# Kernel tuning notes

Hardware: AMD Instinct MI355X
Metric: run time of the kernel (lower is better)

The kernel has to match this reference:

```python
import jax, jax.numpy as jnp
import numpy as np

N_NODES = 50000


def gcn_conv(x, edge_index, W, b):
    # PyG GCNConv: h = X @ W; add self-loops; sym-normalize; scatter-add to target; + bias
    N = x.shape[0]
    h = x @ W
    src = jnp.concatenate([edge_index[0], jnp.arange(N)])
    dst = jnp.concatenate([edge_index[1], jnp.arange(N)])
    ew = jnp.ones(src.shape[0], dtype=h.dtype)
    deg = jax.ops.segment_sum(ew, dst, num_segments=N)
    dinv = jnp.where(deg > 0, deg ** -0.5, 0.0)
    norm = dinv[src] * ew * dinv[dst]              # [E+N]
    msg = h[src] * norm[:, None]                   # gather + scale
    out = jax.ops.segment_sum(msg, dst, num_segments=N)  # scatter-add
    return out + b


def setup_inputs() -> dict:
    key = jax.random.key(0)
    ks = jax.random.split(key, 8)
    x = jax.random.normal(ks[0], (N_NODES, 128), dtype=jnp.float32)
    edge_index = jax.random.randint(ks[1], (2, 800000), 0, N_NODES)
    W1 = jax.random.normal(ks[2], (128, 96), dtype=jnp.float32) * 0.1
    b1 = jax.random.normal(ks[3], (96,), dtype=jnp.float32) * 0.1
    W_mu = jax.random.normal(ks[4], (96, 64), dtype=jnp.float32) * 0.1
    b_mu = jax.random.normal(ks[5], (64,), dtype=jnp.float32) * 0.1
    W_lv = jax.random.normal(ks[6], (96, 64), dtype=jnp.float32) * 0.1
    b_lv = jax.random.normal(ks[7], (64,), dtype=jnp.float32) * 0.1
    return {"x": x, "edge_index": edge_index, "W1": W1, "b1": b1,
            "W_mu": W_mu, "b_mu": b_mu, "W_lv": W_lv, "b_lv": b_lv}


def reference(x, edge_index, W1, b1, W_mu, b_mu, W_lv, b_lv):
    h = jax.nn.relu(gcn_conv(x, edge_index, W1, b1))
    mu = gcn_conv(h, edge_index, W_mu, b_mu).sum(axis=0, keepdims=True)      # SumAggregation -> [1, out]
    logvar = gcn_conv(h, edge_index, W_lv, b_lv).sum(axis=0, keepdims=True)  # [1, out]
    return (mu, logvar)
```

## Files before the change

### kernel.cpp

```cpp
#include <hip/hip_runtime.h>
#include <hip/hip_fp16.h>


#define NCHUNK 32
#define LOG_NCHUNK 5
#define NSLICE 16
#define SLICE_MAX 3136
#define SORT_T 1024

typedef float v2f __attribute__((ext_vector_type(2)));

__device__ inline void fma4(float4& c, float a, const float4& b) {
    c.x = fmaf(a, b.x, c.x); c.y = fmaf(a, b.y, c.y);
    c.z = fmaf(a, b.z, c.z); c.w = fmaf(a, b.w, c.w);
}

__device__ inline unsigned pk_fp8(float a, float b, float c, float d) {
    int p = __builtin_amdgcn_cvt_pk_fp8_f32(a, b, 0, false);
    p = __builtin_amdgcn_cvt_pk_fp8_f32(c, d, p, true);
    return (unsigned)p;
}

__device__ inline void add_fp8(float4& acc, unsigned u) {
    v2f f;
    f = __builtin_amdgcn_cvt_pk_f32_fp8(u, false); acc.x += f.x; acc.y += f.y;
    f = __builtin_amdgcn_cvt_pk_f32_fp8(u, true);  acc.z += f.x; acc.w += f.y;
}

__launch_bounds__(SORT_T)
__global__ void k_count(const int* __restrict__ dst, unsigned short* __restrict__ pcount,
                        int N, int E, int chunkE, int sliceN) {
    int c = blockIdx.x & (NCHUNK - 1), s = blockIdx.x >> LOG_NCHUNK;
    int nbase = s * sliceN;
    __shared__ int hist[SLICE_MAX];
    for (int j = threadIdx.x; j < sliceN; j += SORT_T) hist[j] = 0;
    __syncthreads();
    int e0 = c * chunkE, e1 = min(e0 + chunkE, E);
    int ne = e1 - e0;
    const int4* d4 = (const int4*)(dst + e0);
    int n4 = ne >> 2;
    for (int i = threadIdx.x; i < n4; i += SORT_T) {
        int4 d = d4[i];
        unsigned q;
        q = (unsigned)(d.x - nbase); if (q < (unsigned)sliceN) atomicAdd(&hist[q], 1);
        q = (unsigned)(d.y - nbase); if (q < (unsigned)sliceN) atomicAdd(&hist[q], 1);
        q = (unsigned)(d.z - nbase); if (q < (unsigned)sliceN) atomicAdd(&hist[q], 1);
        q = (unsigned)(d.w - nbase); if (q < (unsigned)sliceN) atomicAdd(&hist[q], 1);
    }
    if (threadIdx.x < (ne & 3)) {
        int d = dst[e0 + (n4 << 2) + threadIdx.x];
        unsigned q = (unsigned)(d - nbase);
        if (q < (unsigned)sliceN) atomicAdd(&hist[q], 1);
    }
    __syncthreads();
    for (int j = threadIdx.x; j < sliceN; j += SORT_T) {
        int n = nbase + j;
        if (n < N) pcount[(size_t)c * N + n] = (unsigned short)hist[j];
    }
}

__launch_bounds__(256)
__global__ void k_degdinv(const unsigned short* __restrict__ pcount, int* __restrict__ deg,
                          float* __restrict__ dinv, int* __restrict__ blocksum, int N) {
    int tid = threadIdx.x;
    int n = blockIdx.x * 256 + tid;
    int s = 0;
    if (n < N) {
        #pragma unroll
        for (int c = 0; c < NCHUNK; ++c) s += pcount[(size_t)c * N + n];
        deg[n] = s;
        dinv[n] = rsqrtf((float)(s + 1));
    }
    __shared__ int sh[256];
    sh[tid] = s;
    __syncthreads();
    #pragma unroll
    for (int off = 128; off; off >>= 1) {
        if (tid < off) sh[tid] += sh[tid + off];
        __syncthreads();
    }
    if (tid == 0) blocksum[blockIdx.x] = sh[0];
}

__launch_bounds__(256)
__global__ void k_offs(const unsigned short* __restrict__ pcount, int* __restrict__ offs,
                       const int* __restrict__ deg, const int* __restrict__ blocksum,
                       int* __restrict__ rowptr, int N, int E, int nb) {
    int tid = threadIdx.x;
    __shared__ int sh[256];
    int bs = (tid < nb && tid < (int)blockIdx.x) ? blocksum[tid] : 0;
    sh[tid] = bs;
    __syncthreads();
    #pragma unroll
    for (int off = 128; off; off >>= 1) {
        if (tid < off) sh[tid] += sh[tid + off];
        __syncthreads();
    }
    int blockoff = sh[0];
    __syncthreads();
    int n = blockIdx.x * 256 + tid;
    int v = (n < N) ? deg[n] : 0;
    sh[tid] = v;
    __syncthreads();
    for (int off = 1; off < 256; off <<= 1) {
        int t = (tid >= off) ? sh[tid - off] : 0;
        __syncthreads();
        sh[tid] += t;
        __syncthreads();
    }
    int run = blockoff + sh[tid] - v;
    if (n < N) {
        rowptr[n] = run;
        #pragma unroll
        for (int c = 0; c < NCHUNK; ++c) {
            size_t ix = (size_t)c * N + n;
            int t = pcount[ix];
            offs[ix] = run;
            run += t;
        }
    }
    if (blockIdx.x == 0 && tid == 0) rowptr[N] = E;
}

__launch_bounds__(SORT_T)
__global__ void k_place(const int* __restrict__ src, const int* __restrict__ dst,
                        const float* __restrict__ dinv, int* __restrict__ offs,
                        int* __restrict__ col, int N, int E, int chunkE, int sliceN) {
    int c = blockIdx.x & (NCHUNK - 1), s = blockIdx.x >> LOG_NCHUNK;
    int nbase = s * sliceN;
    __shared__ int cur[SLICE_MAX];
    __shared__ float rs[SLICE_MAX];
    for (int j = threadIdx.x; j < sliceN; j += SORT_T) {
        int n = nbase + j;
        cur[j] = (n < N) ? offs[(size_t)c * N + n] : 0;
        rs[j] = 0.f;
    }
    __syncthreads();
    int e0 = c * chunkE, e1 = min(e0 + chunkE, E);
    int ne = e1 - e0;
    const int4* s4 = (const int4*)(src + e0);
    const int4* d4 = (const int4*)(dst + e0);
    int n4 = ne >> 2;
    for (int i = threadIdx.x; i < n4; i += SORT_T) {
        int4 sv = s4[i];
        int4 dv = d4[i];
        unsigned qd, qs;
        qd = (unsigned)(dv.x - nbase);
        if (qd < (unsigned)sliceN) { int p = atomicAdd(&cur[qd], 1); col[p] = sv.x; }
        qs = (unsigned)(sv.x - nbase);
        if (qs < (unsigned)sliceN) atomicAdd(&rs[qs], dinv[dv.x]);
        qd = (unsigned)(dv.y - nbase);
        if (qd < (unsigned)sliceN) { int p = atomicAdd(&cur[qd], 1); col[p] = sv.y; }
        qs = (unsigned)(sv.y - nbase);
        if (qs < (unsigned)sliceN) atomicAdd(&rs[qs], dinv[dv.y]);
        qd = (unsigned)(dv.z - nbase);
        if (qd < (unsigned)sliceN) { int p = atomicAdd(&cur[qd], 1); col[p] = sv.z; }
        qs = (unsigned)(sv.z - nbase);
        if (qs < (unsigned)sliceN) atomicAdd(&rs[qs], dinv[dv.z]);
        qd = (unsigned)(dv.w - nbase);
        if (qd < (unsigned)sliceN) { int p = atomicAdd(&cur[qd], 1); col[p] = sv.w; }
        qs = (unsigned)(sv.w - nbase);
        if (qs < (unsigned)sliceN) atomicAdd(&rs[qs], dinv[dv.w]);
    }
    if (threadIdx.x < (ne & 3)) {
        int e = e0 + (n4 << 2) + threadIdx.x;
        int sv = src[e], dv = dst[e];
        unsigned qd = (unsigned)(dv - nbase);
        if (qd < (unsigned)sliceN) { int p = atomicAdd(&cur[qd], 1); col[p] = sv; }
        unsigned qs = (unsigned)(sv - nbase);
        if (qs < (unsigned)sliceN) atomicAdd(&rs[qs], dinv[dv]);
    }
    __syncthreads();
    float* prs = (float*)offs;
    for (int j = threadIdx.x; j < sliceN; j += SORT_T) {
        int n = nbase + j;
        if (n < N) prs[(size_t)c * N + n] = rs[j];
    }
}

__launch_bounds__(256)
__global__ void k_gemm(const float* __restrict__ x, const float* __restrict__ W1,
                       const float* __restrict__ dinv, const float* __restrict__ prs,
                       float* __restrict__ cfac, unsigned* __restrict__ g, int n) {
    __shared__ float Ws[128 * 96];
    int tid = threadIdx.x;
    {
        const float4* wsrc = (const float4*)W1;
        float4* wdst = (float4*)Ws;
        #pragma unroll
        for (int i = 0; i < 12; ++i) wdst[tid + 256 * i] = wsrc[tid + 256 * i];
    }
    {
        int r = blockIdx.x * 128 + tid;
        if (tid < 128 && r < n) {
            float s = 0.f;
            #pragma unroll
            for (int c = 0; c < NCHUNK; ++c) s += prs[(size_t)c * n + r];
            float dv = dinv[r];
            cfac[r] = dv * (dv + s);
        }
    }
    __syncthreads();

    int tx = tid & 7;
    int ty = tid >> 3;
    int rbase = blockIdx.x * 128 + ty * 4;
    const float4* xp[4];
    bool vr[4];
    #pragma unroll
    for (int i = 0; i < 4; ++i) {
        int r = rbase + i;
        vr[i] = r < n;
        xp[i] = (const float4*)(x + (size_t)(vr[i] ? r : 0) * 128);
    }

    float4 acc[4][3];
    #pragma unroll
    for (int i = 0; i < 4; ++i)
        #pragma unroll
        for (int j = 0; j < 3; ++j) acc[i][j] = make_float4(0.f, 0.f, 0.f, 0.f);

    #pragma unroll 2
    for (int k4 = 0; k4 < 32; ++k4) {
        float4 a0 = xp[0][k4];
        float4 a1 = xp[1][k4];
        float4 a2 = xp[2][k4];
        float4 a3 = xp[3][k4];
        #pragma unroll
        for (int kk = 0; kk < 4; ++kk) {
            const float* wrow = &Ws[(k4 * 4 + kk) * 96 + tx * 12];
            float4 b0 = *(const float4*)(wrow);
            float4 b1 = *(const float4*)(wrow + 4);
            float4 b2 = *(const float4*)(wrow + 8);
            float av0 = (kk == 0) ? a0.x : (kk == 1) ? a0.y : (kk == 2) ? a0.z : a0.w;
            float av1 = (kk == 0) ? a1.x : (kk == 1) ? a1.y : (kk == 2) ? a1.z : a1.w;
            float av2 = (kk == 0) ? a2.x : (kk == 1) ? a2.y : (kk == 2) ? a2.z : a2.w;
            float av3 = (kk == 0) ? a3.x : (kk == 1) ? a3.y : (kk == 2) ? a3.z : a3.w;
            fma4(acc[0][0], av0, b0); fma4(acc[0][1], av0, b1); fma4(acc[0][2], av0, b2);
            fma4(acc[1][0], av1, b0); fma4(acc[1][1], av1, b1); fma4(acc[1][2], av1, b2);
            fma4(acc[2][0], av2, b0); fma4(acc[2][1], av2, b1); fma4(acc[2][2], av2, b2);
            fma4(acc[3][0], av3, b0); fma4(acc[3][1], av3, b1); fma4(acc[3][2], av3, b2);
        }
    }

    #pragma unroll
    for (int i = 0; i < 4; ++i) {
        if (!vr[i]) continue;
        int r = rbase + i;
        float dv = dinv[r] * 16.f;
        unsigned* o = g + (size_t)r * 24 + tx * 3;
        float4 t;
        t = acc[i][0]; o[0] = pk_fp8(t.x * dv, t.y * dv, t.z * dv, t.w * dv);
        t = acc[i][1]; o[1] = pk_fp8(t.x * dv, t.y * dv, t.z * dv, t.w * dv);
        t = acc[i][2]; o[2] = pk_fp8(t.x * dv, t.y * dv, t.z * dv, t.w * dv);
    }
}

#define AGG_NODES 16
#define AGG_T (AGG_NODES * 24)
__launch_bounds__(AGG_T)
__global__ void k_agg(const unsigned* __restrict__ g1, const int* __restrict__ col,
                      const int* __restrict__ rowptr, const float* __restrict__ dinv,
                      const float* __restrict__ cfac, const float* __restrict__ b1,
                      float* __restrict__ v_part, int n) {
    int tid = threadIdx.x;
    int nl = tid / 24;
    int ch = tid % 24;
    int d = blockIdx.x * AGG_NODES + nl;

    __shared__ float4 sh[AGG_NODES][24];

    float4 contrib = make_float4(0.f, 0.f, 0.f, 0.f);
    if (d < n) {
        float dds = dinv[d] * 0.0625f;
        int e0 = rowptr[d], e1 = rowptr[d + 1];
        float4 aA = make_float4(0.f, 0.f, 0.f, 0.f);
        float4 aB = make_float4(0.f, 0.f, 0.f, 0.f);
        float4 aC = make_float4(0.f, 0.f, 0.f, 0.f);
        float4 aD = make_float4(0.f, 0.f, 0.f, 0.f);
        int e = e0;
        for (; e + 8 <= e1; e += 8) {
            int s0 = __builtin_nontemporal_load(col + e);
            int s1 = __builtin_nontemporal_load(col + e + 1);
            int s2 = __builtin_nontemporal_load(col + e + 2);
            int s3 = __builtin_nontemporal_load(col + e + 3);
            int s4 = __builtin_nontemporal_load(col + e + 4);
            int s5 = __builtin_nontemporal_load(col + e + 5);
            int s6 = __builtin_nontemporal_load(col + e + 6);
            int s7 = __builtin_nontemporal_load(col + e + 7);
            unsigned u0 = g1[(size_t)s0 * 24 + ch];
            unsigned u1 = g1[(size_t)s1 * 24 + ch];
            unsigned u2 = g1[(size_t)s2 * 24 + ch];
            unsigned u3 = g1[(size_t)s3 * 24 + ch];
            unsigned u4 = g1[(size_t)s4 * 24 + ch];
            unsigned u5 = g1[(size_t)s5 * 24 + ch];
            unsigned u6 = g1[(size_t)s6 * 24 + ch];
            unsigned u7 = g1[(size_t)s7 * 24 + ch];
            add_fp8(aA, u0); add_fp8(aB, u1); add_fp8(aC, u2); add_fp8(aD, u3);
            add_fp8(aA, u4); add_fp8(aB, u5); add_fp8(aC, u6); add_fp8(aD, u7);
        }
        for (; e + 2 <= e1; e += 2) {
            int s0 = __builtin_nontemporal_load(col + e);
            int s1 = __builtin_nontemporal_load(col + e + 1);
            unsigned u0 = g1[(size_t)s0 * 24 + ch];
            unsigned u1 = g1[(size_t)s1 * 24 + ch];
            add_fp8(aA, u0); add_fp8(aB, u1);
        }
        if (e < e1) {
            int s0 = __builtin_nontemporal_load(col + e);
            add_fp8(aC, g1[(size_t)s0 * 24 + ch]);
        }
        add_fp8(aD, g1[(size_t)d * 24 + ch]);
        float4 b1c = ((const float4*)b1)[ch];
        float cd = cfac[d];
        float hx = fmaxf(fmaf(dds, (aA.x + aB.x) + (aC.x + aD.x), b1c.x), 0.f);
        float hy = fmaxf(fmaf(dds, (aA.y + aB.y) + (aC.y + aD.y), b1c.y), 0.f);
        float hz = fmaxf(fmaf(dds, (aA.z + aB.z) + (aC.z + aD.z), b1c.z), 0.f);
        float hw = fmaxf(fmaf(dds, (aA.w + aB.w) + (aC.w + aD.w), b1c.w), 0.f);
        contrib = make_float4(cd * hx, cd * hy, cd * hz, cd * hw);
    }
    sh[nl][ch] = contrib;
    __syncthreads();
    #pragma unroll
    for (int off = 8; off >= 1; off >>= 1) {
        if (nl < off) {
            float4 a = sh[nl][ch];
            float4 b = sh[nl + off][ch];
            a.x += b.x; a.y += b.y; a.z += b.z; a.w += b.w;
            sh[nl][ch] = a;
        }
        __syncthreads();
    }
    if (tid < 24) {
        ((float4*)(v_part + (size_t)blockIdx.x * 96))[tid] = sh[0][tid];
    }
}

__global__ void k_vred(const float* __restrict__ vp, float* __restrict__ v, int nb) {
    int j = blockIdx.x;
    float s = 0.f;
    for (int i = threadIdx.x; i < nb; i += 256) s += vp[(size_t)i * 96 + j];
    __shared__ float sh[256];
    sh[threadIdx.x] = s;
    __syncthreads();
    for (int off = 128; off; off >>= 1) {
        if (threadIdx.x < off) sh[threadIdx.x] += sh[threadIdx.x + off];
        __syncthreads();
    }
    if (threadIdx.x == 0) v[j] = sh[0];
}

__global__ void k_out(const float* __restrict__ v,
                      const float* __restrict__ Wmu, const float* __restrict__ bmu,
                      const float* __restrict__ Wlv, const float* __restrict__ blv,
                      float* __restrict__ out, float nN) {
    int tid = threadIdx.x;
    const float* W = (tid < 64) ? Wmu : Wlv;
    const float* b = (tid < 64) ? bmu : blv;
    int j = tid & 63;
    float s = 0.f;
    #pragma unroll
    for (int k = 0; k < 96; ++k) s = fmaf(v[k], W[k * 64 + j], s);
    out[tid] = s + nN * b[j];
}

extern "C" void kernel_launch(void* const* d_in, const int* in_sizes, int n_in,
                              void* d_out, int out_size, void* d_ws, size_t ws_size,
                              hipStream_t stream) {
    const float* x   = (const float*)d_in[0];
    const int*   ei  = (const int*)d_in[1];
    const float* W1  = (const float*)d_in[2];
    const float* b1  = (const float*)d_in[3];
    const float* Wmu = (const float*)d_in[4];
    const float* bmu = (const float*)d_in[5];
    const float* Wlv = (const float*)d_in[6];
    const float* blv = (const float*)d_in[7];
    float* out = (float*)d_out;

    const int N = in_sizes[0] / 128;
    const int E = in_sizes[1] / 2;
    const int* src = ei;
    const int* dst = ei + E;

    const int chunkE = (((E + NCHUNK - 1) / NCHUNK) + 3) & ~3;
    const int sliceN = (N + NSLICE - 1) / NSLICE;
    const int gN = (N + 255) / 256;

    size_t off = 0;
    auto alloc = [&](size_t bytes) -> char* {
        off = (off + 255) & ~(size_t)255;
        char* p = (char*)d_ws + off;
        off += bytes;
        return p;
    };
    unsigned short* pcount = (unsigned short*)alloc((size_t)NCHUNK * N * 2);
    int*      offsb    = (int*)alloc((size_t)NCHUNK * N * 4);
    int*      rowptr   = (int*)alloc((size_t)(N + 1) * 4);
    int*      col      = (int*)alloc((size_t)E * 4);
    int*      deg      = (int*)alloc((size_t)N * 4);
    float*    dinv     = (float*)alloc((size_t)N * 4);
    float*    cfac     = (float*)alloc((size_t)N * 4);
    int*      blocksum = (int*)alloc((size_t)gN * 4);
    unsigned* g        = (unsigned*)alloc((size_t)N * 96);
    const int nAggBlocks = (N + AGG_NODES - 1) / AGG_NODES;
    float*    v_part   = (float*)alloc((size_t)nAggBlocks * 96 * 4);
    float*    v        = (float*)alloc(96 * 4);

    k_count<<<NCHUNK * NSLICE, SORT_T, 0, stream>>>(dst, pcount, N, E, chunkE, sliceN);
    k_degdinv<<<gN, 256, 0, stream>>>(pcount, deg, dinv, blocksum, N);
    k_offs<<<gN, 256, 0, stream>>>(pcount, offsb, deg, blocksum, rowptr, N, E, gN);
    k_place<<<NCHUNK * NSLICE, SORT_T, 0, stream>>>(src, dst, dinv, offsb, col, N, E, chunkE, sliceN);
    k_gemm<<<(N + 127) / 128, 256, 0, stream>>>(x, W1, dinv, (const float*)offsb, cfac, g, N);
    k_agg<<<nAggBlocks, AGG_T, 0, stream>>>(g, col, rowptr, dinv, cfac, b1, v_part, N);
    k_vred<<<96, 256, 0, stream>>>(v_part, v, nAggBlocks);
    k_out<<<1, 128, 0, stream>>>(v, Wmu, bmu, Wlv, blv, out, (float)N);
}
```

Baseline: 92.20 us.

## Use fp16 MFMA for the first-layer GEMM instead of scalar FMA

Rewrites k_gemm so that X@W1 runs on the 16x16x32 f16 MFMA instructions. W1 is repacked in shared memory into fp16 fragments and x rows are converted to fp16 in registers. The block tile drops from 128 to 64 rows, which doubles the grid. This is meant to cut ALU-bound FMA time, at the cost of fp16 input precision and a per-block cost for repacking W.

Measured after the change: 83.67 us, median of 3. 9.2% less time.

```diff
diff --git a/kernel.cpp b/kernel.cpp
--- a/kernel.cpp
+++ b/kernel.cpp
@@ -9,10 +9,12 @@
 #define SORT_T 1024
 
 typedef float v2f __attribute__((ext_vector_type(2)));
-
-__device__ inline void fma4(float4& c, float a, const float4& b) {
-    c.x = fmaf(a, b.x, c.x); c.y = fmaf(a, b.y, c.y);
-    c.z = fmaf(a, b.z, c.z); c.w = fmaf(a, b.w, c.w);
+typedef float f32x4 __attribute__((ext_vector_type(4)));
+typedef _Float16 half8 __attribute__((ext_vector_type(8)));
+
+__device__ inline unsigned f2h(float a, float b) {
+    __half2 h = __floats2half2_rn(a, b);
+    return *reinterpret_cast<unsigned*>(&h);
 }
 
 __device__ inline unsigned pk_fp8(float a, float b, float c, float d) {
@@ -183,6 +185,7 @@
                        const float* __restrict__ dinv, const float* __restrict__ prs,
                        float* __restrict__ cfac, unsigned* __restrict__ g, int n) {
     __shared__ float Ws[128 * 96];
+    __shared__ uint4 Whu4[24 * 64];
     int tid = threadIdx.x;
     {
         const float4* wsrc = (const float4*)W1;
@@ -191,8 +194,8 @@
         for (int i = 0; i < 12; ++i) wdst[tid + 256 * i] = wsrc[tid + 256 * i];
     }
     {
-        int r = blockIdx.x * 128 + tid;
-        if (tid < 128 && r < n) {
+        int r = blockIdx.x * 64 + tid;
+        if (tid < 64 && r < n) {
             float s = 0.f;
             #pragma unroll
             for (int c = 0; c < NCHUNK; ++c) s += prs[(size_t)c * n + r];
@@ -202,57 +205,53 @@
     }
     __syncthreads();
 
-    int tx = tid & 7;
-    int ty = tid >> 3;
-    int rbase = blockIdx.x * 128 + ty * 4;
-    const float4* xp[4];
-    bool vr[4];
-    #pragma unroll
-    for (int i = 0; i < 4; ++i) {
-        int r = rbase + i;
-        vr[i] = r < n;
-        xp[i] = (const float4*)(x + (size_t)(vr[i] ? r : 0) * 128);
-    }
-
-    float4 acc[4][3];
-    #pragma unroll
-    for (int i = 0; i < 4; ++i)
+    for (int idx = tid; idx < 24 * 64; idx += 256) {
+        int lane = idx & 63;
+        int frag = idx >> 6;
+        int ks = frag / 6, ct = frag - ks * 6;
+        int k0 = ks * 32 + (lane >> 4) * 8;
+        int c = ct * 16 + (lane & 15);
+        const float* wsp = Ws + (size_t)k0 * 96 + c;
+        Whu4[idx] = make_uint4(f2h(wsp[0],   wsp[96]),
+                               f2h(wsp[192], wsp[288]),
+                               f2h(wsp[384], wsp[480]),
+                               f2h(wsp[576], wsp[672]));
+    }
+    __syncthreads();
+
+    int wid = tid >> 6, lane = tid & 63;
+    int xrow = blockIdx.x * 64 + wid * 16 + (lane & 15);
+    bool vrow = xrow < n;
+    const float4* xp = (const float4*)(x + (size_t)(vrow ? xrow : 0) * 128);
+
+    f32x4 acc[6];
+    #pragma unroll
+    for (int ct = 0; ct < 6; ++ct) acc[ct] = (f32x4){0.f, 0.f, 0.f, 0.f};
+
+    #pragma unroll
+    for (int ks = 0; ks < 4; ++ks) {
+        float4 xa = xp[ks * 8 + (lane >> 4) * 2];
+        float4 xb = xp[ks * 8 + (lane >> 4) * 2 + 1];
+        half8 bf;
+        bf[0] = (_Float16)xa.x; bf[1] = (_Float16)xa.y;
+        bf[2] = (_Float16)xa.z; bf[3] = (_Float16)xa.w;
+        bf[4] = (_Float16)xb.x; bf[5] = (_Float16)xb.y;
+        bf[6] = (_Float16)xb.z; bf[7] = (_Float16)xb.w;
         #pragma unroll
-        for (int j = 0; j < 3; ++j) acc[i][j] = make_float4(0.f, 0.f, 0.f, 0.f);
-
-    #pragma unroll 2
-    for (int k4 = 0; k4 < 32; ++k4) {
-        float4 a0 = xp[0][k4];
-        float4 a1 = xp[1][k4];
-        float4 a2 = xp[2][k4];
-        float4 a3 = xp[3][k4];
+        for (int ct = 0; ct < 6; ++ct) {
+            half8 af = *reinterpret_cast<const half8*>(&Whu4[(ks * 6 + ct) * 64 + lane]);
+            acc[ct] = __builtin_amdgcn_mfma_f32_16x16x32_f16(af, bf, acc[ct], 0, 0, 0);
+        }
+    }
+
+    if (vrow) {
+        float dv = dinv[xrow] * 16.f;
+        unsigned* o = g + (size_t)xrow * 24 + (lane >> 4);
         #pragma unroll
-        for (int kk = 0; kk < 4; ++kk) {
-            const float* wrow = &Ws[(k4 * 4 + kk) * 96 + tx * 12];
-            float4 b0 = *(const float4*)(wrow);
-            float4 b1 = *(const float4*)(wrow + 4);
-            float4 b2 = *(const float4*)(wrow + 8);
-            float av0 = (kk == 0) ? a0.x : (kk == 1) ? a0.y : (kk == 2) ? a0.z : a0.w;
-            float av1 = (kk == 0) ? a1.x : (kk == 1) ? a1.y : (kk == 2) ? a1.z : a1.w;
-            float av2 = (kk == 0) ? a2.x : (kk == 1) ? a2.y : (kk == 2) ? a2.z : a2.w;
-            float av3 = (kk == 0) ? a3.x : (kk == 1) ? a3.y : (kk == 2) ? a3.z : a3.w;
-            fma4(acc[0][0], av0, b0); fma4(acc[0][1], av0, b1); fma4(acc[0][2], av0, b2);
-            fma4(acc[1][0], av1, b0); fma4(acc[1][1], av1, b1); fma4(acc[1][2], av1, b2);
-            fma4(acc[2][0], av2, b0); fma4(acc[2][1], av2, b1); fma4(acc[2][2], av2, b2);
-            fma4(acc[3][0], av3, b0); fma4(acc[3][1], av3, b1); fma4(acc[3][2], av3, b2);
-        }
-    }
-
-    #pragma unroll
-    for (int i = 0; i < 4; ++i) {
-        if (!vr[i]) continue;
-        int r = rbase + i;
-        float dv = dinv[r] * 16.f;
-        unsigned* o = g + (size_t)r * 24 + tx * 3;
-        float4 t;
-        t = acc[i][0]; o[0] = pk_fp8(t.x * dv, t.y * dv, t.z * dv, t.w * dv);
-        t = acc[i][1]; o[1] = pk_fp8(t.x * dv, t.y * dv, t.z * dv, t.w * dv);
-        t = acc[i][2]; o[2] = pk_fp8(t.x * dv, t.y * dv, t.z * dv, t.w * dv);
+        for (int ct = 0; ct < 6; ++ct) {
+            o[ct * 4] = pk_fp8(acc[ct][0] * dv, acc[ct][1] * dv,
+                               acc[ct][2] * dv, acc[ct][3] * dv);
+        }
     }
 }
 
@@ -410,7 +409,7 @@
     k_degdinv<<<gN, 256, 0, stream>>>(pcount, deg, dinv, blocksum, N);
     k_offs<<<gN, 256, 0, stream>>>(pcount, offsb, deg, blocksum, rowptr, N, E, gN);
     k_place<<<NCHUNK * NSLICE, SORT_T, 0, stream>>>(src, dst, dinv, offsb, col, N, E, chunkE, sliceN);
-    k_gemm<<<(N + 127) / 128, 256, 0, stream>>>(x, W1, dinv, (const float*)offsb, cfac, g, N);
+    k_gemm<<<(N + 63) / 64, 256, 0, stream>>>(x, W1, dinv, (const float*)offsb, cfac, g, N);
     k_agg<<<nAggBlocks, AGG_T, 0, stream>>>(g, col, rowptr, dinv, cfac, b1, v_part, N);
     k_vred<<<96, 256, 0, stream>>>(v_part, v, nAggBlocks);
     k_out<<<1, 128, 0, stream>>>(v, Wmu, bmu, Wlv, blv, out, (float)N);
```
